# Kernel optimization log

Hardware: AMD Instinct MI355X
Metric: run time of the kernel (lower is better)

## Reference

```python
import jax, jax.numpy as jnp
import numpy as np

N, NA, LAYERS = 8, 4, 4
NTOT = N + NA
DIM = 2 ** NTOT
B = 1024

# Diagonal of the fixed CZ brick layer (CZ is diagonal, so one elementwise pass per layer).
# Qubit 0 is the most-significant bit of the state index (tensorcircuit convention).
def _cz_diag():
    idx = np.arange(DIM)
    bits = (idx[None, :] >> (NTOT - 1 - np.arange(NTOT)[:, None])) & 1  # [NTOT, DIM]
    par = np.zeros(DIM, dtype=np.int64)
    for i in range(NTOT // 2):
        par += bits[2 * i] * bits[2 * i + 1]
    for i in range((NTOT - 1) // 2):
        par += bits[2 * i + 1] * bits[2 * i + 2]
    return jnp.asarray(1.0 - 2.0 * (par % 2), dtype=jnp.complex64)

CZ_DIAG = _cz_diag()

def _apply_1q(state, U, q):
    # state: [B, DIM]; apply 2x2 unitary U on qubit q (batched over samples)
    l, r = 2 ** q, 2 ** (NTOT - q - 1)
    s = state.reshape(-1, l, 2, r)
    return jnp.einsum('ij,bljr->blir', U, s).reshape(-1, DIM)

def _back_circuit(state, params):
    # hardware-efficient ansatz: per layer RX,RY on every qubit, then CZ bricks
    for lay in range(LAYERS):
        off = 2 * NTOT * lay
        for q in range(NTOT):
            th = params[off + q] * 0.5
            c = jnp.cos(th).astype(jnp.complex64)
            ms = (-1j) * jnp.sin(th).astype(jnp.complex64)
            Rx = jnp.stack([jnp.stack([c, ms]), jnp.stack([ms, c])])
            state = _apply_1q(state, Rx, q)
            th = params[off + NTOT + q] * 0.5
            c, s = jnp.cos(th), jnp.sin(th)
            Ry = jnp.stack([jnp.stack([c, -s]), jnp.stack([s, c])]).astype(jnp.complex64)
            state = _apply_1q(state, Ry, q)
        state = state * CZ_DIAG
    return state

def setup_inputs() -> dict:
    key = jax.random.key(0)
    k1, k2, k3, k4 = jax.random.split(key, 4)
    return {
        'inputs_re': jax.random.normal(k1, (B, DIM), jnp.float32),
        'inputs_im': jax.random.normal(k2, (B, DIM), jnp.float32),
        'params': jax.random.normal(k3, (2 * NTOT * LAYERS,), jnp.float32),
        'u': jax.random.uniform(k4, (B,), jnp.float32),
    }

def reference(inputs_re, inputs_im, params, u):
    state = (inputs_re + 1j * inputs_im).astype(jnp.complex64)
    full = _back_circuit(state, params)                      # [B, 2^n_tot]
    s3 = full.reshape(B, 2 ** NA, 2 ** N)                    # [B, 2^na, 2^n]
    probs = jnp.sum(s3.real ** 2 + s3.imag ** 2, axis=2)     # ancilla outcome probs
    cdf = jnp.cumsum(probs, axis=1)
    thresh = u * cdf[:, -1]                                  # inverse-CDF multinomial
    m = jnp.argmax(cdf >= thresh[:, None], axis=1)           # [B] sampled outcome
    post = s3[jnp.arange(B), m]                              # [B, 2^n] collapsed state
    norm = jnp.sqrt(jnp.sum(post.real ** 2 + post.imag ** 2, axis=1, keepdims=True))
    post = post / norm
    return jnp.stack([post.real, post.imag], axis=-1)        # [B, 2^n, 2]
```

## Files before the change

kernel.cpp:

```cpp
#include <hip/hip_runtime.h>
#include <math.h>

#define NTOT   12
#define DIM    4096
#define LAYERS 4
#define NB     1024
#define SPAD   4608

typedef float v2f __attribute__((ext_vector_type(2)));

template<int G>
__device__ __forceinline__ void gate_pk(v2f (&x)[16], v2f P1, v2f P2) {
#pragma unroll
    for (int p = 0; p < 8; ++p) {
        const int j0 = ((p >> G) << (G + 1)) | (p & ((1 << G) - 1));
        const int j1 = j0 | (1 << G);
        const v2f x0 = x[j0], x1 = x[j1];
        v2f t, u;
        asm("v_pk_mul_f32 %0, %1, %2 op_sel:[1,1] op_sel_hi:[1,0] neg_hi:[1,0]"
            : "=v"(t) : "v"(P2), "v"(x1));
        asm("v_pk_fma_f32 %0, %1, %2, %0 op_sel:[1,0,0] op_sel_hi:[1,1,1] neg_lo:[1,0,0] neg_hi:[1,0,0]"
            : "+v"(t) : "v"(P1), "v"(x1));
        asm("v_pk_fma_f32 %0, %1, %2, %0 op_sel:[0,1,0] op_sel_hi:[0,0,1] neg_lo:[1,0,0]"
            : "+v"(t) : "v"(P2), "v"(x0));
        asm("v_pk_fma_f32 %0, %1, %2, %0 op_sel:[0,0,0] op_sel_hi:[0,1,1]"
            : "+v"(t) : "v"(P1), "v"(x0));
        asm("v_pk_mul_f32 %0, %1, %2 op_sel:[0,1] op_sel_hi:[0,0] neg_hi:[1,0]"
            : "=v"(u) : "v"(P2), "v"(x1));
        asm("v_pk_fma_f32 %0, %1, %2, %0 op_sel:[0,0,0] op_sel_hi:[0,1,1]"
            : "+v"(u) : "v"(P1), "v"(x1));
        asm("v_pk_fma_f32 %0, %1, %2, %0 op_sel:[1,1,0] op_sel_hi:[1,0,1] neg_hi:[1,0,0]"
            : "+v"(u) : "v"(P2), "v"(x0));
        asm("v_pk_fma_f32 %0, %1, %2, %0 op_sel:[1,0,0] op_sel_hi:[1,1,1]"
            : "+v"(u) : "v"(P1), "v"(x0));
        x[j0] = t; x[j1] = u;
    }
}

__device__ __forceinline__ void apply4(v2f (&x)[16], const float4* gco, int base) {
    float4 c;
    c = gco[base + 3]; gate_pk<0>(x, (v2f){c.x, c.y}, (v2f){c.z, c.w});
    c = gco[base + 2]; gate_pk<1>(x, (v2f){c.x, c.y}, (v2f){c.z, c.w});
    c = gco[base + 1]; gate_pk<2>(x, (v2f){c.x, c.y}, (v2f){c.z, c.w});
    c = gco[base + 0]; gate_pk<3>(x, (v2f){c.x, c.y}, (v2f){c.z, c.w});
}

__device__ __forceinline__ void applyCZ(v2f (&x)[16], const int (&sw)[16]) {
#pragma unroll
    for (int j = 0; j < 16; ++j) {
        x[j].x = __uint_as_float(__float_as_uint(x[j].x) ^ sw[j]);
        x[j].y = __uint_as_float(__float_as_uint(x[j].y) ^ sw[j]);
    }
}

__global__ __launch_bounds__(256, 4) void qddpm_kernel(
    const float* __restrict__ in_re,
    const float* __restrict__ in_im,
    const float* __restrict__ params,
    const float* __restrict__ uu,
    float* __restrict__ out)
{
    __shared__ v2f    S[SPAD];
    __shared__ float4 gco[48];
    __shared__ float  sprob[16];

    const int b = blockIdx.x;
    const int t = threadIdx.x;
    const float uval = uu[b];

    const int baseA = t + 2 * (t >> 4);
    const int baseB = (t >> 4) * 288 + (t & 15);
    const int baseC = t * 18;

    v2f x[16];

    {
        const float4* re4 = (const float4*)(in_re + (size_t)b * DIM + t * 16);
        const float4* im4 = (const float4*)(in_im + (size_t)b * DIM + t * 16);
#pragma unroll
        for (int q = 0; q < 4; ++q) {
            const float4 vr = re4[q];
            const float4 vi = im4[q];
            x[4 * q + 0] = (v2f){vr.x, vi.x};
            x[4 * q + 1] = (v2f){vr.y, vi.y};
            x[4 * q + 2] = (v2f){vr.z, vi.z};
            x[4 * q + 3] = (v2f){vr.w, vi.w};
        }
    }
    if (t < 48) {
        const int lay = t / 12, q = t - lay * 12;
        float c1, s1, c2, s2;
        sincosf(params[lay * 24 + q] * 0.5f, &s1, &c1);
        sincosf(params[lay * 24 + 12 + q] * 0.5f, &s2, &c2);
        gco[t] = make_float4(c1 * c2, c1 * s2, s1 * s2, s1 * c2);
    }

    int swA[16], swC[16];
#pragma unroll
    for (int j = 0; j < 16; ++j) {
        const int iC = t * 16 + j;
        swC[j] = (__popc(iC & (iC >> 1) & 0x7FF) & 1) << 31;
        const int iA = j * 256 + t;
        swA[j] = (__popc(iA & (iA >> 1) & 0x7FF) & 1) << 31;
    }

    __syncthreads();

    apply4(x, gco, 0 * 12 + 8);
    {
        float4* dst = (float4*)(S + baseC);
#pragma unroll
        for (int q = 0; q < 8; ++q)
            dst[q] = make_float4(x[2 * q].x, x[2 * q].y, x[2 * q + 1].x, x[2 * q + 1].y);
    }
    __syncthreads();

#pragma unroll
    for (int j = 0; j < 16; ++j) x[j] = S[baseB + 18 * j];
    apply4(x, gco, 0 * 12 + 4);
#pragma unroll
    for (int j = 0; j < 16; ++j) S[baseB + 18 * j] = x[j];
    __syncthreads();

#pragma unroll
    for (int j = 0; j < 16; ++j) x[j] = S[baseA + 288 * j];
    apply4(x, gco, 0 * 12 + 0);
    applyCZ(x, swA);
    apply4(x, gco, 1 * 12 + 0);
#pragma unroll
    for (int j = 0; j < 16; ++j) S[baseA + 288 * j] = x[j];
    __syncthreads();

#pragma unroll
    for (int j = 0; j < 16; ++j) x[j] = S[baseB + 18 * j];
    apply4(x, gco, 1 * 12 + 4);
#pragma unroll
    for (int j = 0; j < 16; ++j) S[baseB + 18 * j] = x[j];
    __syncthreads();

    {
        const float4* src = (const float4*)(S + baseC);
#pragma unroll
        for (int q = 0; q < 8; ++q) {
            const float4 v = src[q];
            x[2 * q]     = (v2f){v.x, v.y};
            x[2 * q + 1] = (v2f){v.z, v.w};
        }
    }
    apply4(x, gco, 1 * 12 + 8);
    applyCZ(x, swC);
    apply4(x, gco, 2 * 12 + 8);
    {
        float4* dst = (float4*)(S + baseC);
#pragma unroll
        for (int q = 0; q < 8; ++q)
            dst[q] = make_float4(x[2 * q].x, x[2 * q].y, x[2 * q + 1].x, x[2 * q + 1].y);
    }
    __syncthreads();

#pragma unroll
    for (int j = 0; j < 16; ++j) x[j] = S[baseB + 18 * j];
    apply4(x, gco, 2 * 12 + 4);
#pragma unroll
    for (int j = 0; j < 16; ++j) S[baseB + 18 * j] = x[j];
    __syncthreads();

#pragma unroll
    for (int j = 0; j < 16; ++j) x[j] = S[baseA + 288 * j];
    apply4(x, gco, 2 * 12 + 0);
    applyCZ(x, swA);
    apply4(x, gco, 3 * 12 + 0);
#pragma unroll
    for (int j = 0; j < 16; ++j) S[baseA + 288 * j] = x[j];
    __syncthreads();

#pragma unroll
    for (int j = 0; j < 16; ++j) x[j] = S[baseB + 18 * j];
    apply4(x, gco, 3 * 12 + 4);
#pragma unroll
    for (int j = 0; j < 16; ++j) S[baseB + 18 * j] = x[j];
    __syncthreads();

    {
        const float4* src = (const float4*)(S + baseC);
#pragma unroll
        for (int q = 0; q < 8; ++q) {
            const float4 v = src[q];
            x[2 * q]     = (v2f){v.x, v.y};
            x[2 * q + 1] = (v2f){v.z, v.w};
        }
    }
    apply4(x, gco, 3 * 12 + 8);
    applyCZ(x, swC);
    {
        v2f acc2 = (v2f){0.0f, 0.0f};
#pragma unroll
        for (int j = 0; j < 16; ++j) acc2 += x[j] * x[j];
        float4* dst = (float4*)(S + baseC);
#pragma unroll
        for (int q = 0; q < 8; ++q)
            dst[q] = make_float4(x[2 * q].x, x[2 * q].y, x[2 * q + 1].x, x[2 * q + 1].y);
        float partial = acc2.x + acc2.y;
#pragma unroll
        for (int o = 8; o > 0; o >>= 1)
            partial += __shfl_down(partial, o, 16);
        if ((t & 15) == 0) sprob[t >> 4] = partial;
    }
    __syncthreads();

    {
        float cdf[16];
        float a = 0.0f;
#pragma unroll
        for (int i = 0; i < 16; ++i) { a += sprob[i]; cdf[i] = a; }
        const float thresh = uval * a;
        int m = 0;
#pragma unroll
        for (int i = 15; i >= 0; --i) { if (cdf[i] >= thresh) m = i; }
        const float rn = 1.0f / sqrtf(sprob[m]);
        const v2f amp = S[baseA + 288 * m];
        ((float2*)out)[(size_t)b * 256 + t] = make_float2(amp.x * rn, amp.y * rn);
    }
}

extern "C" void kernel_launch(void* const* d_in, const int* in_sizes, int n_in,
                              void* d_out, int out_size, void* d_ws, size_t ws_size,
                              hipStream_t stream) {
    const float* in_re  = (const float*)d_in[0];
    const float* in_im  = (const float*)d_in[1];
    const float* params = (const float*)d_in[2];
    const float* u      = (const float*)d_in[3];
    float* out = (float*)d_out;
    qddpm_kernel<<<NB, 256, 0, stream>>>(in_re, in_im, params, u, out);
}
```

Baseline: 107.4 us.

## Simulate each sample in one wavefront with 64 amplitudes per lane

Restructures the kernel so one 64-lane wavefront owns a whole 4096-amplitude state, 64 complex amplitudes per lane in registers. Six-qubit gate groups are applied between XOR-swizzled LDS transposes, with only wave-level waits and no block barriers. Gate coefficients are broadcast with readlane instead of shared memory, and CZ signs are computed from constexpr parity. The ancilla reduction uses shuffles and only the selected lanes write output. The cost is very high register pressure (128 VGPRs for state alone) and only 512 blocks of two waves each, which may hurt occupancy and latency hiding.

```diff
diff --git a/kernel.cpp b/kernel.cpp
--- a/kernel.cpp
+++ b/kernel.cpp
@@ -1,18 +1,22 @@
 #include <hip/hip_runtime.h>
 #include <math.h>
 
-#define NTOT   12
 #define DIM    4096
-#define LAYERS 4
 #define NB     1024
-#define SPAD   4608
+#define WPB    2
+#define NBLK   (NB / WPB)
 
 typedef float v2f __attribute__((ext_vector_type(2)));
 
+__host__ __device__ constexpr int czP5(int j) {
+    return (((j >> 0) & (j >> 1)) ^ ((j >> 1) & (j >> 2)) ^ ((j >> 2) & (j >> 3)) ^
+            ((j >> 3) & (j >> 4)) ^ ((j >> 4) & (j >> 5))) & 1;
+}
+
 template<int G>
-__device__ __forceinline__ void gate_pk(v2f (&x)[16], v2f P1, v2f P2) {
-#pragma unroll
-    for (int p = 0; p < 8; ++p) {
+__device__ __forceinline__ void gate_pk(v2f (&x)[64], v2f P1, v2f P2) {
+#pragma unroll
+    for (int p = 0; p < 32; ++p) {
         const int j0 = ((p >> G) << (G + 1)) | (p & ((1 << G) - 1));
         const int j1 = j0 | (1 << G);
         const v2f x0 = x[j0], x1 = x[j1];
@@ -37,48 +41,43 @@
     }
 }
 
-__device__ __forceinline__ void apply4(v2f (&x)[16], const float4* gco, int base) {
-    float4 c;
-    c = gco[base + 3]; gate_pk<0>(x, (v2f){c.x, c.y}, (v2f){c.z, c.w});
-    c = gco[base + 2]; gate_pk<1>(x, (v2f){c.x, c.y}, (v2f){c.z, c.w});
-    c = gco[base + 1]; gate_pk<2>(x, (v2f){c.x, c.y}, (v2f){c.z, c.w});
-    c = gco[base + 0]; gate_pk<3>(x, (v2f){c.x, c.y}, (v2f){c.z, c.w});
-}
-
-__device__ __forceinline__ void applyCZ(v2f (&x)[16], const int (&sw)[16]) {
-#pragma unroll
-    for (int j = 0; j < 16; ++j) {
-        x[j].x = __uint_as_float(__float_as_uint(x[j].x) ^ sw[j]);
-        x[j].y = __uint_as_float(__float_as_uint(x[j].y) ^ sw[j]);
-    }
-}
-
-__global__ __launch_bounds__(256, 4) void qddpm_kernel(
+template<bool XL>
+__device__ __forceinline__ void applyCZ(v2f (&x)[64], unsigned w0, unsigned w0s,
+                                        unsigned w1, unsigned w1s) {
+#pragma unroll
+    for (int j = 0; j < 64; ++j) {
+        const bool hi = XL ? ((j & 32) != 0) : ((j & 1) != 0);
+        const unsigned wo = czP5(j) ? (hi ? w1s : w0s) : (hi ? w1 : w0);
+        x[j].x = __uint_as_float(__float_as_uint(x[j].x) ^ wo);
+        x[j].y = __uint_as_float(__float_as_uint(x[j].y) ^ wo);
+    }
+}
+
+#define WAVEWAIT() asm volatile("s_waitcnt lgkmcnt(0)" ::: "memory")
+
+__global__ __launch_bounds__(128, 1) void qddpm_kernel(
     const float* __restrict__ in_re,
     const float* __restrict__ in_im,
     const float* __restrict__ params,
     const float* __restrict__ uu,
     float* __restrict__ out)
 {
-    __shared__ v2f    S[SPAD];
-    __shared__ float4 gco[48];
-    __shared__ float  sprob[16];
-
-    const int b = blockIdx.x;
-    const int t = threadIdx.x;
+    __shared__ v2f S[WPB * DIM];
+
+    const int tid  = threadIdx.x;
+    const int w    = tid >> 6;
+    const int lane = tid & 63;
+    const int b    = blockIdx.x * WPB + w;
+    v2f* Sw = S + w * DIM;
+
     const float uval = uu[b];
 
-    const int baseA = t + 2 * (t >> 4);
-    const int baseB = (t >> 4) * 288 + (t & 15);
-    const int baseC = t * 18;
-
-    v2f x[16];
-
+    v2f x[64];
     {
-        const float4* re4 = (const float4*)(in_re + (size_t)b * DIM + t * 16);
-        const float4* im4 = (const float4*)(in_im + (size_t)b * DIM + t * 16);
-#pragma unroll
-        for (int q = 0; q < 4; ++q) {
+        const float4* re4 = (const float4*)(in_re + (size_t)b * DIM + lane * 64);
+        const float4* im4 = (const float4*)(in_im + (size_t)b * DIM + lane * 64);
+#pragma unroll
+        for (int q = 0; q < 16; ++q) {
             const float4 vr = re4[q];
             const float4 vi = im4[q];
             x[4 * q + 0] = (v2f){vr.x, vi.x};
@@ -87,139 +86,115 @@
             x[4 * q + 3] = (v2f){vr.w, vi.w};
         }
     }
-    if (t < 48) {
-        const int lay = t / 12, q = t - lay * 12;
+
+    float gv0 = 0.f, gv1 = 0.f, gv2 = 0.f, gv3 = 0.f;
+    if (lane < 48) {
+        const int lay = lane / 12, q = lane - lay * 12;
         float c1, s1, c2, s2;
         sincosf(params[lay * 24 + q] * 0.5f, &s1, &c1);
         sincosf(params[lay * 24 + 12 + q] * 0.5f, &s2, &c2);
-        gco[t] = make_float4(c1 * c2, c1 * s2, s1 * s2, s1 * c2);
-    }
-
-    int swA[16], swC[16];
-#pragma unroll
-    for (int j = 0; j < 16; ++j) {
-        const int iC = t * 16 + j;
-        swC[j] = (__popc(iC & (iC >> 1) & 0x7FF) & 1) << 31;
-        const int iA = j * 256 + t;
-        swA[j] = (__popc(iA & (iA >> 1) & 0x7FF) & 1) << 31;
-    }
-
-    __syncthreads();
-
-    apply4(x, gco, 0 * 12 + 8);
-    {
-        float4* dst = (float4*)(S + baseC);
-#pragma unroll
-        for (int q = 0; q < 8; ++q)
-            dst[q] = make_float4(x[2 * q].x, x[2 * q].y, x[2 * q + 1].x, x[2 * q + 1].y);
-    }
-    __syncthreads();
-
-#pragma unroll
-    for (int j = 0; j < 16; ++j) x[j] = S[baseB + 18 * j];
-    apply4(x, gco, 0 * 12 + 4);
-#pragma unroll
-    for (int j = 0; j < 16; ++j) S[baseB + 18 * j] = x[j];
-    __syncthreads();
-
-#pragma unroll
-    for (int j = 0; j < 16; ++j) x[j] = S[baseA + 288 * j];
-    apply4(x, gco, 0 * 12 + 0);
-    applyCZ(x, swA);
-    apply4(x, gco, 1 * 12 + 0);
-#pragma unroll
-    for (int j = 0; j < 16; ++j) S[baseA + 288 * j] = x[j];
-    __syncthreads();
-
-#pragma unroll
-    for (int j = 0; j < 16; ++j) x[j] = S[baseB + 18 * j];
-    apply4(x, gco, 1 * 12 + 4);
-#pragma unroll
-    for (int j = 0; j < 16; ++j) S[baseB + 18 * j] = x[j];
-    __syncthreads();
-
-    {
-        const float4* src = (const float4*)(S + baseC);
-#pragma unroll
-        for (int q = 0; q < 8; ++q) {
-            const float4 v = src[q];
-            x[2 * q]     = (v2f){v.x, v.y};
-            x[2 * q + 1] = (v2f){v.z, v.w};
+        gv0 = c1 * c2; gv1 = c1 * s2; gv2 = s1 * s2; gv3 = s1 * c2;
+    }
+
+    const unsigned SGN = 0x80000000u;
+    const unsigned ct  = (unsigned)czP5(lane) << 31;
+    const unsigned sx1 = ct ^ ((unsigned)(lane & 1) << 31);
+    const unsigned sy1 = ct ^ ((unsigned)((lane >> 5) & 1) << 31);
+
+#pragma clang loop unroll(disable)
+    for (int h = 0; h < 8; ++h) {
+        const int  l   = h >> 1;
+        const int  hm4 = h & 3;
+        const bool isX = (hm4 == 0) || (hm4 == 3);
+        const int  cb  = l * 12 + (isX ? 6 : 0);
+
+        v2f P1, P2;
+#define GETP(GL) \
+        P1.x = __int_as_float(__builtin_amdgcn_readlane(__float_as_int(gv0), (GL))); \
+        P1.y = __int_as_float(__builtin_amdgcn_readlane(__float_as_int(gv1), (GL))); \
+        P2.x = __int_as_float(__builtin_amdgcn_readlane(__float_as_int(gv2), (GL))); \
+        P2.y = __int_as_float(__builtin_amdgcn_readlane(__float_as_int(gv3), (GL)))
+        GETP(cb + 5); gate_pk<0>(x, P1, P2);
+        GETP(cb + 4); gate_pk<1>(x, P1, P2);
+        GETP(cb + 3); gate_pk<2>(x, P1, P2);
+        GETP(cb + 2); gate_pk<3>(x, P1, P2);
+        GETP(cb + 1); gate_pk<4>(x, P1, P2);
+        GETP(cb + 0); gate_pk<5>(x, P1, P2);
+#undef GETP
+
+        if (h & 1) {
+            if ((h >> 1) & 1) applyCZ<true >(x, ct, ct ^ SGN, sx1, sx1 ^ SGN);
+            else              applyCZ<false>(x, ct, ct ^ SGN, sy1, sy1 ^ SGN);
+        } else {
+            WAVEWAIT();
+            if (((h >> 1) & 1) == 0) {
+                {
+                    float4* wb = (float4*)((char*)Sw + lane * 512);
+                    const unsigned hs = (unsigned)(lane & 30) >> 1;
+#pragma unroll
+                    for (int c = 0; c < 64; c += 2)
+                        wb[(unsigned)(c >> 1) ^ hs] =
+                            make_float4(x[c].x, x[c].y, x[c + 1].x, x[c + 1].y);
+                }
+                WAVEWAIT();
+#pragma unroll
+                for (int r = 0; r < 64; ++r) {
+                    const v2f* rb = (const v2f*)((char*)Sw +
+                        (((unsigned)(lane ^ (r & 30))) << 3));
+                    x[r] = rb[r * 64];
+                }
+            } else {
+#pragma unroll
+                for (int r = 0; r < 64; ++r) {
+                    v2f* wb = (v2f*)((char*)Sw +
+                        (((unsigned)(lane ^ (r & 30))) << 3));
+                    wb[r * 64] = x[r];
+                }
+                WAVEWAIT();
+                {
+                    const float4* rb = (const float4*)((char*)Sw + lane * 512);
+                    const unsigned hs = (unsigned)(lane & 30) >> 1;
+#pragma unroll
+                    for (int c = 0; c < 64; c += 2) {
+                        const float4 v = rb[(unsigned)(c >> 1) ^ hs];
+                        x[c]     = (v2f){v.x, v.y};
+                        x[c + 1] = (v2f){v.z, v.w};
+                    }
+                }
+            }
         }
     }
-    apply4(x, gco, 1 * 12 + 8);
-    applyCZ(x, swC);
-    apply4(x, gco, 2 * 12 + 8);
-    {
-        float4* dst = (float4*)(S + baseC);
-#pragma unroll
-        for (int q = 0; q < 8; ++q)
-            dst[q] = make_float4(x[2 * q].x, x[2 * q].y, x[2 * q + 1].x, x[2 * q + 1].y);
-    }
-    __syncthreads();
-
-#pragma unroll
-    for (int j = 0; j < 16; ++j) x[j] = S[baseB + 18 * j];
-    apply4(x, gco, 2 * 12 + 4);
-#pragma unroll
-    for (int j = 0; j < 16; ++j) S[baseB + 18 * j] = x[j];
-    __syncthreads();
-
-#pragma unroll
-    for (int j = 0; j < 16; ++j) x[j] = S[baseA + 288 * j];
-    apply4(x, gco, 2 * 12 + 0);
-    applyCZ(x, swA);
-    apply4(x, gco, 3 * 12 + 0);
-#pragma unroll
-    for (int j = 0; j < 16; ++j) S[baseA + 288 * j] = x[j];
-    __syncthreads();
-
-#pragma unroll
-    for (int j = 0; j < 16; ++j) x[j] = S[baseB + 18 * j];
-    apply4(x, gco, 3 * 12 + 4);
-#pragma unroll
-    for (int j = 0; j < 16; ++j) S[baseB + 18 * j] = x[j];
-    __syncthreads();
-
-    {
-        const float4* src = (const float4*)(S + baseC);
-#pragma unroll
-        for (int q = 0; q < 8; ++q) {
-            const float4 v = src[q];
-            x[2 * q]     = (v2f){v.x, v.y};
-            x[2 * q + 1] = (v2f){v.z, v.w};
-        }
-    }
-    apply4(x, gco, 3 * 12 + 8);
-    applyCZ(x, swC);
-    {
-        v2f acc2 = (v2f){0.0f, 0.0f};
-#pragma unroll
-        for (int j = 0; j < 16; ++j) acc2 += x[j] * x[j];
-        float4* dst = (float4*)(S + baseC);
-#pragma unroll
-        for (int q = 0; q < 8; ++q)
-            dst[q] = make_float4(x[2 * q].x, x[2 * q].y, x[2 * q + 1].x, x[2 * q + 1].y);
-        float partial = acc2.x + acc2.y;
-#pragma unroll
-        for (int o = 8; o > 0; o >>= 1)
-            partial += __shfl_down(partial, o, 16);
-        if ((t & 15) == 0) sprob[t >> 4] = partial;
-    }
-    __syncthreads();
-
-    {
-        float cdf[16];
-        float a = 0.0f;
-#pragma unroll
-        for (int i = 0; i < 16; ++i) { a += sprob[i]; cdf[i] = a; }
-        const float thresh = uval * a;
-        int m = 0;
-#pragma unroll
-        for (int i = 15; i >= 0; --i) { if (cdf[i] >= thresh) m = i; }
-        const float rn = 1.0f / sqrtf(sprob[m]);
-        const v2f amp = S[baseA + 288 * m];
-        ((float2*)out)[(size_t)b * 256 + t] = make_float2(amp.x * rn, amp.y * rn);
+
+    v2f acc = (v2f){0.f, 0.f};
+#pragma unroll
+    for (int j = 0; j < 64; ++j) acc += x[j] * x[j];
+    float partial = acc.x + acc.y;
+    partial += __shfl_xor(partial, 1);
+    partial += __shfl_xor(partial, 2);
+
+    float pr[16];
+#pragma unroll
+    for (int g = 0; g < 16; ++g) pr[g] = __shfl(partial, g * 4);
+
+    float cdf[16];
+    float a = 0.f;
+#pragma unroll
+    for (int g = 0; g < 16; ++g) { a += pr[g]; cdf[g] = a; }
+    const float thresh = uval * a;
+    int m = 0;
+#pragma unroll
+    for (int g = 15; g >= 0; --g) { if (cdf[g] >= thresh) m = g; }
+    float pm = pr[0];
+#pragma unroll
+    for (int g = 1; g < 16; ++g) { if (m == g) pm = pr[g]; }
+    const float rn = 1.0f / sqrtf(pm);
+
+    if ((lane >> 2) == m) {
+        float4* o = (float4*)((float2*)out + (size_t)b * 256 + (lane & 3) * 64);
+#pragma unroll
+        for (int q = 0; q < 32; ++q)
+            o[q] = make_float4(x[2 * q].x * rn, x[2 * q].y * rn,
+                               x[2 * q + 1].x * rn, x[2 * q + 1].y * rn);
     }
 }
 
@@ -231,5 +206,5 @@
     const float* params = (const float*)d_in[2];
     const float* u      = (const float*)d_in[3];
     float* out = (float*)d_out;
-    qddpm_kernel<<<NB, 256, 0, stream>>>(in_re, in_im, params, u, out);
-}
+    qddpm_kernel<<<NBLK, 128, 0, stream>>>(in_re, in_im, params, u, out);
+}
```

After: 113.3 us. +5.5%, slower.
